# Optimization experiments

Measured on AMD Instinct MI355X. Metric: run time of the kernel, lower is better.

Reference implementation:

```python
import jax, jax.numpy as jnp
import numpy as np

T, B, H = 2048, 8, 1024


def setup_inputs() -> dict:
    key = jax.random.key(0)
    ks = jax.random.split(key, 4)
    scale = 1.0 / np.sqrt(H)
    x = jax.random.normal(ks[0], (T, B, H), dtype=jnp.float32)
    W_q = jax.random.normal(ks[1], (H, H), dtype=jnp.float32) * scale
    b_q = jnp.zeros((H,), dtype=jnp.float32)
    beta_raw = jax.random.normal(ks[2], (H,), dtype=jnp.float32)
    W_fc = jax.random.normal(ks[3], (H, H), dtype=jnp.float32) * scale
    b_fc = jnp.zeros((H,), dtype=jnp.float32)
    return {"x": x, "W_q": W_q, "b_q": b_q, "beta_raw": beta_raw,
            "W_fc": W_fc, "b_fc": b_fc}


def reference(x, W_q, b_q, beta_raw, W_fc, b_fc):
    # Per-neuron learned leak in (0,1)
    beta = jax.nn.sigmoid(beta_raw)  # (H,)
    # Input (q) projection: (T,B,H) @ (H,H)^T
    q = jnp.einsum('tbh,oh->tbo', x, W_q) + b_q  # (T,B,H)
    # Leaky integration m_t = beta * m_{t-1} + q_t as an associative scan over T
    a = jnp.broadcast_to(beta, q.shape)  # (T,B,H)

    def combine(c1, c2):
        a1, m1 = c1
        a2, m2 = c2
        return (a1 * a2, a2 * m1 + m2)

    _, m = jax.lax.associative_scan(combine, (a, q), axis=0)  # (T,B,H)
    # Linear + ReLU
    h = jnp.einsum('tbh,oh->tbo', m, W_fc) + b_fc
    return jax.nn.relu(h)
```

## Files before the change

### kernel.cpp

```cpp
#include <hip/hip_runtime.h>
#include <stdint.h>

typedef unsigned short u16;
typedef __bf16 bf16x8 __attribute__((ext_vector_type(8)));
typedef float f32x4 __attribute__((ext_vector_type(4)));

__device__ __forceinline__ u16 f2bf(float f) {
  union { float f; uint32_t u; } x; x.f = f;
  uint32_t u = x.u;
  u += 0x7fffu + ((u >> 16) & 1u);
  return (u16)(u >> 16);
}
__device__ __forceinline__ float bf2f(uint32_t lo16) {
  union { uint32_t u; float f; } x; x.u = lo16 << 16; return x.f;
}

__device__ __forceinline__ void async_load16(const u16* g, u16* l) {
  __builtin_amdgcn_global_load_lds(
      (const __attribute__((address_space(1))) void*)g,
      (__attribute__((address_space(3))) void*)l,
      16, 0, 0);
}

__global__ __launch_bounds__(256) void prep_all(const float* __restrict__ x,
                                                const float* __restrict__ Wq,
                                                const float* __restrict__ Wfc,
                                                const float* __restrict__ braw,
                                                u16* __restrict__ xb,
                                                u16* __restrict__ wqb,
                                                u16* __restrict__ wfcb,
                                                float* __restrict__ beta) {
  int gid = blockIdx.x * 256 + threadIdx.x;
  if (gid < 1024) beta[gid] = 1.0f / (1.0f + expf(-braw[gid]));
  if (gid < 131072) {
    const int HH = 1024 * 1024;
    int i = gid * 16;
    const float* src = (i < HH) ? (Wq + i) : (Wfc + (i - HH));
    u16* dst = (i < HH) ? (wqb + i) : (wfcb + (i - HH));
#pragma unroll
    for (int c = 0; c < 4; c++) {
      float4 v = *(const float4*)(src + c * 4);
      ushort4 o = {f2bf(v.x), f2bf(v.y), f2bf(v.z), f2bf(v.w)};
      *(ushort4*)(dst + c * 4) = o;
    }
  }
  {
    int i = gid * 8;
    float4 a = *(const float4*)(x + i);
    float4 b = *(const float4*)(x + i + 4);
    ushort4 o0 = {f2bf(a.x), f2bf(a.y), f2bf(a.z), f2bf(a.w)};
    ushort4 o1 = {f2bf(b.x), f2bf(b.y), f2bf(b.z), f2bf(b.w)};
    *(ushort4*)(xb + i) = o0;
    *(ushort4*)(xb + i + 4) = o1;
  }
}

template <int RELU, int OUTBF>
__global__ __launch_bounds__(512, 2) void gemm256(const u16* __restrict__ A,
                                                  const u16* __restrict__ B,
                                                  const float* __restrict__ bias,
                                                  void* __restrict__ Cout,
                                                  int M, int N, int K) {
  __shared__ u16 lds[4][2][256 * 32];

  const int tid  = threadIdx.x;
  const int lane = tid & 63;
  const int wid  = tid >> 6;
  const int wr   = (wid >> 2) * 128;
  const int wc   = (wid & 3) * 64;

  const int bid    = blockIdx.x;
  const int tile_m = (bid >> 2) * 256;
  const int tile_n = (bid & 3) * 256;

  const int srow    = tid >> 2;
  const int schunk  = (tid & 3) ^ ((srow >> 1) & 3);
  const u16* gA = A + (size_t)(tile_m + srow) * K + schunk * 8;
  const u16* gB = B + (size_t)(tile_n + srow) * K + schunk * 8;
  const size_t half_stride = (size_t)128 * K;

#define STAGE(slot, kt)                                                   \
  do {                                                                    \
    const size_t k0 = (size_t)(kt) * 32;                                  \
    async_load16(gA + k0,               &lds[slot][0][wid * 512]);        \
    async_load16(gA + k0 + half_stride, &lds[slot][0][4096 + wid * 512]); \
    async_load16(gB + k0,               &lds[slot][1][wid * 512]);        \
    async_load16(gB + k0 + half_stride, &lds[slot][1][4096 + wid * 512]); \
  } while (0)

  f32x4 acc[8][4];
#pragma unroll
  for (int i = 0; i < 8; i++)
#pragma unroll
    for (int j = 0; j < 4; j++) acc[i][j] = (f32x4){0.f, 0.f, 0.f, 0.f};

  const int lrow = lane & 15;
  const int kq   = lane >> 4;
  const int kc   = (lrow >> 1) & 3;
  const int coff = ((kq ^ kc) << 3);

  const int NKT = K >> 5;

  STAGE(0, 0);
  if (NKT > 1) STAGE(1, 1);
  if (NKT > 2) STAGE(2, 2);
  if (NKT > 2)      asm volatile("s_waitcnt vmcnt(8)" ::: "memory");
  else if (NKT > 1) asm volatile("s_waitcnt vmcnt(4)" ::: "memory");
  else              asm volatile("s_waitcnt vmcnt(0)" ::: "memory");
  __builtin_amdgcn_s_barrier();

  for (int kt = 0; kt < NKT; ++kt) {
    const int slot = kt & 3;
    const u16* As = &lds[slot][0][0];
    const u16* Bs = &lds[slot][1][0];

    bf16x8 a[8], b[4];
#pragma unroll
    for (int i = 0; i < 8; i++)
      a[i] = *(const bf16x8*)&As[(wr + i * 16 + lrow) * 32 + coff];
#pragma unroll
    for (int j = 0; j < 4; j++)
      b[j] = *(const bf16x8*)&Bs[(wc + j * 16 + lrow) * 32 + coff];

    if (kt + 3 < NKT) STAGE((kt + 3) & 3, kt + 3);

    __builtin_amdgcn_s_setprio(1);
#pragma unroll
    for (int i = 0; i < 8; i++)
#pragma unroll
      for (int j = 0; j < 4; j++)
        acc[i][j] = __builtin_amdgcn_mfma_f32_16x16x32_bf16(a[i], b[j], acc[i][j], 0, 0, 0);
    __builtin_amdgcn_s_setprio(0);

    const int ahead = NKT - 1 - kt;
    if (ahead >= 3) {
      asm volatile("s_waitcnt vmcnt(8)" ::: "memory");
      __builtin_amdgcn_s_barrier();
    } else if (ahead == 2) {
      asm volatile("s_waitcnt vmcnt(4)" ::: "memory");
      __builtin_amdgcn_s_barrier();
    } else if (ahead == 1) {
      asm volatile("s_waitcnt vmcnt(0)" ::: "memory");
      __builtin_amdgcn_s_barrier();
    }
  }
#undef STAGE

  const int crow = (lane >> 4) << 2;
  const int ccol = lane & 15;
#pragma unroll
  for (int i = 0; i < 8; i++) {
#pragma unroll
    for (int j = 0; j < 4; j++) {
      const int gm = tile_m + wr + i * 16 + crow;
      const int gn = tile_n + wc + j * 16 + ccol;
      const float bv = bias[gn];
#pragma unroll
      for (int r = 0; r < 4; r++) {
        float v = acc[i][j][r] + bv;
        if (RELU) v = fmaxf(v, 0.f);
        if (OUTBF) ((u16*)Cout)[(size_t)(gm + r) * N + gn] = f2bf(v);
        else       ((float*)Cout)[(size_t)(gm + r) * N + gn] = v;
      }
    }
  }
}

#define NCH 8192
#define SEG 32
#define NSEG 64

__global__ __launch_bounds__(256) void scan_carry(const uint2* __restrict__ qb,
                                                  float* __restrict__ carry,
                                                  const float* __restrict__ beta_arr) {
  int tid = blockIdx.x * 256 + threadIdx.x;
  int seg = tid >> 11;
  int cq  = tid & 2047;
  int h0  = (cq * 4) & 1023;
  float b0 = beta_arr[h0], b1 = beta_arr[h0 + 1], b2 = beta_arr[h0 + 2], b3 = beta_arr[h0 + 3];
  const uint2* p = qb + (size_t)seg * SEG * 2048 + cq;
  float m0 = 0.f, m1 = 0.f, m2 = 0.f, m3 = 0.f;
#pragma unroll 8
  for (int t = 0; t < SEG; t++) {
    uint2 v = p[(size_t)t * 2048];
    m0 = fmaf(b0, m0, bf2f(v.x & 0xffffu));
    m1 = fmaf(b1, m1, bf2f(v.x >> 16));
    m2 = fmaf(b2, m2, bf2f(v.y & 0xffffu));
    m3 = fmaf(b3, m3, bf2f(v.y >> 16));
  }
  *(float4*)&carry[(size_t)seg * NCH + cq * 4] = make_float4(m0, m1, m2, m3);
}

__global__ __launch_bounds__(256) void scan_fuse(const uint2* __restrict__ qb,
                                                 const float4* __restrict__ carry4,
                                                 const float* __restrict__ beta_arr,
                                                 uint2* __restrict__ mb) {
  const int tid = blockIdx.x * 256 + threadIdx.x;
  const int seg = tid >> 11;
  const int cq  = tid & 2047;
  const int h0  = (cq * 4) & 1023;
  const float b0 = beta_arr[h0], b1 = beta_arr[h0 + 1];
  const float b2 = beta_arr[h0 + 2], b3 = beta_arr[h0 + 3];
  float s0 = b0, s1 = b1, s2 = b2, s3 = b3;
#pragma unroll
  for (int i = 0; i < 5; i++) { s0 *= s0; s1 *= s1; s2 *= s2; s3 *= s3; }
  float m0 = 0.f, m1 = 0.f, m2 = 0.f, m3 = 0.f;
  const float4* cp = carry4 + cq;
  for (int s = 0; s < seg; s++) {
    float4 c = cp[(size_t)s * 2048];
    m0 = fmaf(s0, m0, c.x); m1 = fmaf(s1, m1, c.y);
    m2 = fmaf(s2, m2, c.z); m3 = fmaf(s3, m3, c.w);
  }
  const uint2* p = qb + (size_t)seg * SEG * 2048 + cq;
  uint2* o = mb + (size_t)seg * SEG * 2048 + cq;
#pragma unroll 8
  for (int t = 0; t < SEG; t++) {
    uint2 v = p[(size_t)t * 2048];
    m0 = fmaf(b0, m0, bf2f(v.x & 0xffffu));
    m1 = fmaf(b1, m1, bf2f(v.x >> 16));
    m2 = fmaf(b2, m2, bf2f(v.y & 0xffffu));
    m3 = fmaf(b3, m3, bf2f(v.y >> 16));
    uint2 w;
    w.x = (uint32_t)f2bf(m0) | ((uint32_t)f2bf(m1) << 16);
    w.y = (uint32_t)f2bf(m2) | ((uint32_t)f2bf(m3) << 16);
    o[(size_t)t * 2048] = w;
  }
}

extern "C" void kernel_launch(void* const* d_in, const int* in_sizes, int n_in,
                              void* d_out, int out_size, void* d_ws, size_t ws_size,
                              hipStream_t stream) {
  const float* x        = (const float*)d_in[0];
  const float* W_q      = (const float*)d_in[1];
  const float* b_q      = (const float*)d_in[2];
  const float* beta_raw = (const float*)d_in[3];
  const float* W_fc     = (const float*)d_in[4];
  const float* b_fc     = (const float*)d_in[5];

  const int H = 1024;
  const int M = 2048 * 8;
  const size_t MH = (size_t)M * H;

  char* ws = (char*)d_ws;
  u16* x_bf    = (u16*)ws;  ws += MH * 2;
  u16* q_bf    = (u16*)ws;  ws += MH * 2;
  u16* m_bf    = (u16*)ws;  ws += MH * 2;
  u16* wq_bf   = (u16*)ws;  ws += (size_t)H * H * 2;
  u16* wfc_bf  = (u16*)ws;  ws += (size_t)H * H * 2;
  float* beta  = (float*)ws; ws += 4096;
  float* carry = (float*)ws; ws += (size_t)NSEG * NCH * 4;

  prep_all<<<(int)(MH / 8 / 256), 256, 0, stream>>>(x, W_q, W_fc, beta_raw,
                                                    x_bf, wq_bf, wfc_bf, beta);

  gemm256<0, 1><<<256, 512, 0, stream>>>(x_bf, wq_bf, b_q, q_bf, M, H, H);

  scan_carry<<<NSEG * (NCH / 4) / 256, 256, 0, stream>>>((const uint2*)q_bf, carry, beta);
  scan_fuse<<<NSEG * (NCH / 4) / 256, 256, 0, stream>>>((const uint2*)q_bf,
                                                        (const float4*)carry, beta,
                                                        (uint2*)m_bf);

  gemm256<1, 0><<<256, 512, 0, stream>>>(m_bf, wfc_bf, b_fc, d_out, M, H, H);
}
```

Baseline: 240.1 us.

## Restructure GEMM main loop into 64-wide K tiles with interleaved sub-phase staging

The GEMM kernel moves from a 4-slot K=32 pipeline to a double-buffered K=64 pipeline. Each K tile is split into four phases that interleave A-fragment LDS reads, async global-to-LDS staging of the next A and B tiles, and MFMA blocks. The aim is to hide global and LDS latency behind the MFMA work. It also uses an 8-chunk XOR swizzle suited to 64-wide rows, and remaps block IDs so that tiles sharing an A row block land on the same XCD for better L2 reuse. The cost is many more barriers per iteration, and the tighter staging schedule could stall if loads do not arrive in time.

```diff
diff --git a/kernel.cpp b/kernel.cpp
--- a/kernel.cpp
+++ b/kernel.cpp
@@ -61,7 +61,7 @@
                                                   const float* __restrict__ bias,
                                                   void* __restrict__ Cout,
                                                   int M, int N, int K) {
-  __shared__ u16 lds[4][2][256 * 32];
+  __shared__ u16 lds[2][2][256 * 64];
 
   const int tid  = threadIdx.x;
   const int lane = tid & 63;
@@ -70,22 +70,29 @@
   const int wc   = (wid & 3) * 64;
 
   const int bid    = blockIdx.x;
-  const int tile_m = (bid >> 2) * 256;
-  const int tile_n = (bid & 3) * 256;
-
-  const int srow    = tid >> 2;
-  const int schunk  = (tid & 3) ^ ((srow >> 1) & 3);
-  const u16* gA = A + (size_t)(tile_m + srow) * K + schunk * 8;
-  const u16* gB = B + (size_t)(tile_n + srow) * K + schunk * 8;
-  const size_t half_stride = (size_t)128 * K;
-
-#define STAGE(slot, kt)                                                   \
-  do {                                                                    \
-    const size_t k0 = (size_t)(kt) * 32;                                  \
-    async_load16(gA + k0,               &lds[slot][0][wid * 512]);        \
-    async_load16(gA + k0 + half_stride, &lds[slot][0][4096 + wid * 512]); \
-    async_load16(gB + k0,               &lds[slot][1][wid * 512]);        \
-    async_load16(gB + k0 + half_stride, &lds[slot][1][4096 + wid * 512]); \
+  const int xcd    = bid & 7;
+  const int idx    = bid >> 3;
+  const int tile_m = ((xcd << 3) | (idx >> 2)) * 256;
+  const int tile_n = (idx & 3) * 256;
+
+  const int srow = tid >> 3;
+  const int sch  = (tid & 7) ^ (srow & 7);
+  const u16* gA = A + (size_t)(tile_m + srow) * K + sch * 8;
+  const u16* gB = B + (size_t)(tile_n + srow) * K + sch * 8;
+
+#define STAGE_A(bp, h, kt)                                              \
+  do {                                                                  \
+    const u16* _s = gA + (size_t)(h) * 128 * K + (size_t)(kt) * 64;     \
+    async_load16(_s,                 &(bp)[(h) * 8192 + wid * 512]);    \
+    async_load16(_s + (size_t)64 * K,                                   \
+                 &(bp)[(h) * 8192 + 4096 + wid * 512]);                 \
+  } while (0)
+#define STAGE_B(bp, h, kt)                                              \
+  do {                                                                  \
+    const u16* _s = gB + (size_t)(h) * 128 * K + (size_t)(kt) * 64;     \
+    async_load16(_s,                 &(bp)[(h) * 8192 + wid * 512]);    \
+    async_load16(_s + (size_t)64 * K,                                   \
+                 &(bp)[(h) * 8192 + 4096 + wid * 512]);                 \
   } while (0)
 
   f32x4 acc[8][4];
@@ -96,55 +103,136 @@
 
   const int lrow = lane & 15;
   const int kq   = lane >> 4;
-  const int kc   = (lrow >> 1) & 3;
-  const int coff = ((kq ^ kc) << 3);
-
-  const int NKT = K >> 5;
-
-  STAGE(0, 0);
-  if (NKT > 1) STAGE(1, 1);
-  if (NKT > 2) STAGE(2, 2);
-  if (NKT > 2)      asm volatile("s_waitcnt vmcnt(8)" ::: "memory");
-  else if (NKT > 1) asm volatile("s_waitcnt vmcnt(4)" ::: "memory");
-  else              asm volatile("s_waitcnt vmcnt(0)" ::: "memory");
+  const int x0   = ((kq)     ^ (lrow & 7)) << 3;
+  const int x1   = ((kq + 4) ^ (lrow & 7)) << 3;
+
+  const int NT = K >> 6;
+
+  {
+    u16* b0A = &lds[0][0][0];
+    u16* b0B = &lds[0][1][0];
+    STAGE_B(b0B, 0, 0);
+    STAGE_B(b0B, 1, 0);
+    STAGE_A(b0A, 0, 0);
+    STAGE_A(b0A, 1, 0);
+    if (NT > 1) {
+      u16* b1B = &lds[1][1][0];
+      STAGE_B(b1B, 0, 1);
+      STAGE_B(b1B, 1, 1);
+      asm volatile("s_waitcnt vmcnt(4)" ::: "memory");
+    } else {
+      asm volatile("s_waitcnt vmcnt(0)" ::: "memory");
+    }
+  }
   __builtin_amdgcn_s_barrier();
 
-  for (int kt = 0; kt < NKT; ++kt) {
-    const int slot = kt & 3;
-    const u16* As = &lds[slot][0][0];
-    const u16* Bs = &lds[slot][1][0];
-
-    bf16x8 a[8], b[4];
-#pragma unroll
-    for (int i = 0; i < 8; i++)
-      a[i] = *(const bf16x8*)&As[(wr + i * 16 + lrow) * 32 + coff];
-#pragma unroll
-    for (int j = 0; j < 4; j++)
-      b[j] = *(const bf16x8*)&Bs[(wc + j * 16 + lrow) * 32 + coff];
-
-    if (kt + 3 < NKT) STAGE((kt + 3) & 3, kt + 3);
-
+  bf16x8 bfr[4][2];
+
+  for (int t = 0; t < NT; ++t) {
+    const int buf = t & 1;
+    const u16* As = &lds[buf][0][0];
+    const u16* Bs = &lds[buf][1][0];
+    u16* nA = &lds[buf ^ 1][0][0];
+    u16* cB = &lds[buf][1][0];
+
+#pragma unroll
+    for (int n = 0; n < 4; n++) {
+      bfr[n][0] = *(const bf16x8*)&Bs[(wc + n * 16 + lrow) * 64 + x0];
+      bfr[n][1] = *(const bf16x8*)&Bs[(wc + n * 16 + lrow) * 64 + x1];
+    }
+    bf16x8 a0k0 = *(const bf16x8*)&As[(wr + 0 * 16 + lrow) * 64 + x0];
+    bf16x8 a0k1 = *(const bf16x8*)&As[(wr + 0 * 16 + lrow) * 64 + x1];
+    bf16x8 a1k0 = *(const bf16x8*)&As[(wr + 1 * 16 + lrow) * 64 + x0];
+    bf16x8 a1k1 = *(const bf16x8*)&As[(wr + 1 * 16 + lrow) * 64 + x1];
+    if (t + 1 < NT) { STAGE_A(nA, 0, t + 1); STAGE_A(nA, 1, t + 1); }
+    __builtin_amdgcn_s_barrier();
+    asm volatile("s_waitcnt lgkmcnt(0)" ::: "memory");
+    __builtin_amdgcn_sched_barrier(0);
     __builtin_amdgcn_s_setprio(1);
 #pragma unroll
-    for (int i = 0; i < 8; i++)
-#pragma unroll
-      for (int j = 0; j < 4; j++)
-        acc[i][j] = __builtin_amdgcn_mfma_f32_16x16x32_bf16(a[i], b[j], acc[i][j], 0, 0, 0);
+    for (int n = 0; n < 4; n++) {
+      acc[0][n] = __builtin_amdgcn_mfma_f32_16x16x32_bf16(a0k0, bfr[n][0], acc[0][n], 0, 0, 0);
+      acc[1][n] = __builtin_amdgcn_mfma_f32_16x16x32_bf16(a1k0, bfr[n][0], acc[1][n], 0, 0, 0);
+    }
+#pragma unroll
+    for (int n = 0; n < 4; n++) {
+      acc[0][n] = __builtin_amdgcn_mfma_f32_16x16x32_bf16(a0k1, bfr[n][1], acc[0][n], 0, 0, 0);
+      acc[1][n] = __builtin_amdgcn_mfma_f32_16x16x32_bf16(a1k1, bfr[n][1], acc[1][n], 0, 0, 0);
+    }
     __builtin_amdgcn_s_setprio(0);
-
-    const int ahead = NKT - 1 - kt;
-    if (ahead >= 3) {
-      asm volatile("s_waitcnt vmcnt(8)" ::: "memory");
-      __builtin_amdgcn_s_barrier();
-    } else if (ahead == 2) {
-      asm volatile("s_waitcnt vmcnt(4)" ::: "memory");
-      __builtin_amdgcn_s_barrier();
-    } else if (ahead == 1) {
-      asm volatile("s_waitcnt vmcnt(0)" ::: "memory");
-      __builtin_amdgcn_s_barrier();
-    }
-  }
-#undef STAGE
+    __builtin_amdgcn_s_barrier();
+
+    a0k0 = *(const bf16x8*)&As[(wr + 2 * 16 + lrow) * 64 + x0];
+    a0k1 = *(const bf16x8*)&As[(wr + 2 * 16 + lrow) * 64 + x1];
+    a1k0 = *(const bf16x8*)&As[(wr + 3 * 16 + lrow) * 64 + x0];
+    a1k1 = *(const bf16x8*)&As[(wr + 3 * 16 + lrow) * 64 + x1];
+    if (t + 2 < NT) STAGE_B(cB, 0, t + 2);
+    __builtin_amdgcn_s_barrier();
+    asm volatile("s_waitcnt lgkmcnt(0)" ::: "memory");
+    __builtin_amdgcn_sched_barrier(0);
+    __builtin_amdgcn_s_setprio(1);
+#pragma unroll
+    for (int n = 0; n < 4; n++) {
+      acc[2][n] = __builtin_amdgcn_mfma_f32_16x16x32_bf16(a0k0, bfr[n][0], acc[2][n], 0, 0, 0);
+      acc[3][n] = __builtin_amdgcn_mfma_f32_16x16x32_bf16(a1k0, bfr[n][0], acc[3][n], 0, 0, 0);
+    }
+#pragma unroll
+    for (int n = 0; n < 4; n++) {
+      acc[2][n] = __builtin_amdgcn_mfma_f32_16x16x32_bf16(a0k1, bfr[n][1], acc[2][n], 0, 0, 0);
+      acc[3][n] = __builtin_amdgcn_mfma_f32_16x16x32_bf16(a1k1, bfr[n][1], acc[3][n], 0, 0, 0);
+    }
+    __builtin_amdgcn_s_setprio(0);
+    __builtin_amdgcn_s_barrier();
+
+    a0k0 = *(const bf16x8*)&As[(wr + 4 * 16 + lrow) * 64 + x0];
+    a0k1 = *(const bf16x8*)&As[(wr + 4 * 16 + lrow) * 64 + x1];
+    a1k0 = *(const bf16x8*)&As[(wr + 5 * 16 + lrow) * 64 + x0];
+    a1k1 = *(const bf16x8*)&As[(wr + 5 * 16 + lrow) * 64 + x1];
+    if (t + 2 < NT) STAGE_B(cB, 1, t + 2);
+    __builtin_amdgcn_s_barrier();
+    asm volatile("s_waitcnt lgkmcnt(0)" ::: "memory");
+    __builtin_amdgcn_sched_barrier(0);
+    __builtin_amdgcn_s_setprio(1);
+#pragma unroll
+    for (int n = 0; n < 4; n++) {
+      acc[4][n] = __builtin_amdgcn_mfma_f32_16x16x32_bf16(a0k0, bfr[n][0], acc[4][n], 0, 0, 0);
+      acc[5][n] = __builtin_amdgcn_mfma_f32_16x16x32_bf16(a1k0, bfr[n][0], acc[5][n], 0, 0, 0);
+    }
+#pragma unroll
+    for (int n = 0; n < 4; n++) {
+      acc[4][n] = __builtin_amdgcn_mfma_f32_16x16x32_bf16(a0k1, bfr[n][1], acc[4][n], 0, 0, 0);
+      acc[5][n] = __builtin_amdgcn_mfma_f32_16x16x32_bf16(a1k1, bfr[n][1], acc[5][n], 0, 0, 0);
+    }
+    __builtin_amdgcn_s_setprio(0);
+    __builtin_amdgcn_s_barrier();
+
+    a0k0 = *(const bf16x8*)&As[(wr + 6 * 16 + lrow) * 64 + x0];
+    a0k1 = *(const bf16x8*)&As[(wr + 6 * 16 + lrow) * 64 + x1];
+    a1k0 = *(const bf16x8*)&As[(wr + 7 * 16 + lrow) * 64 + x0];
+    a1k1 = *(const bf16x8*)&As[(wr + 7 * 16 + lrow) * 64 + x1];
+    if (t < NT - 1) {
+      if (t + 2 < NT) asm volatile("s_waitcnt vmcnt(4)" ::: "memory");
+      else            asm volatile("s_waitcnt vmcnt(0)" ::: "memory");
+    }
+    __builtin_amdgcn_s_barrier();
+    asm volatile("s_waitcnt lgkmcnt(0)" ::: "memory");
+    __builtin_amdgcn_sched_barrier(0);
+    __builtin_amdgcn_s_setprio(1);
+#pragma unroll
+    for (int n = 0; n < 4; n++) {
+      acc[6][n] = __builtin_amdgcn_mfma_f32_16x16x32_bf16(a0k0, bfr[n][0], acc[6][n], 0, 0, 0);
+      acc[7][n] = __builtin_amdgcn_mfma_f32_16x16x32_bf16(a1k0, bfr[n][0], acc[7][n], 0, 0, 0);
+    }
+#pragma unroll
+    for (int n = 0; n < 4; n++) {
+      acc[6][n] = __builtin_amdgcn_mfma_f32_16x16x32_bf16(a0k1, bfr[n][1], acc[6][n], 0, 0, 0);
+      acc[7][n] = __builtin_amdgcn_mfma_f32_16x16x32_bf16(a1k1, bfr[n][1], acc[7][n], 0, 0, 0);
+    }
+    __builtin_amdgcn_s_setprio(0);
+    if (t < NT - 1) __builtin_amdgcn_s_barrier();
+  }
+#undef STAGE_A
+#undef STAGE_B
 
   const int crow = (lane >> 4) << 2;
   const int ccol = lane & 15;
```

Result: no change. 237.7 us (-1.0%).

## Load B fragments directly to registers, double-buffer A in LDS with BK=64, XCD tile remap

Applied to the files above, without the earlier changes.

Restructures the bf16 GEMM main loop. The B operand is now prefetched straight from global memory into registers, one step ahead, and no longer goes through LDS. The A tile is double-buffered in LDS with a 64-wide K step and an 8-way XOR swizzle, where before there was a 4-slot ring with K=32. Block IDs are remapped so that each XCD gets a contiguous range of M tiles, which should improve L2 locality. The aim is to cut LDS traffic and barriers per K step, at the cost of redundant global/L2 reads of B across waves and a shallower prefetch depth.

```diff
diff --git a/kernel.cpp b/kernel.cpp
--- a/kernel.cpp
+++ b/kernel.cpp
@@ -61,7 +61,7 @@
                                                   const float* __restrict__ bias,
                                                   void* __restrict__ Cout,
                                                   int M, int N, int K) {
-  __shared__ u16 lds[4][2][256 * 32];
+  __shared__ u16 lds[2][256 * 64];
 
   const int tid  = threadIdx.x;
   const int lane = tid & 63;
@@ -70,22 +70,22 @@
   const int wc   = (wid & 3) * 64;
 
   const int bid    = blockIdx.x;
-  const int tile_m = (bid >> 2) * 256;
-  const int tile_n = (bid & 3) * 256;
-
-  const int srow    = tid >> 2;
-  const int schunk  = (tid & 3) ^ ((srow >> 1) & 3);
-  const u16* gA = A + (size_t)(tile_m + srow) * K + schunk * 8;
-  const u16* gB = B + (size_t)(tile_n + srow) * K + schunk * 8;
-  const size_t half_stride = (size_t)128 * K;
-
-#define STAGE(slot, kt)                                                   \
-  do {                                                                    \
-    const size_t k0 = (size_t)(kt) * 32;                                  \
-    async_load16(gA + k0,               &lds[slot][0][wid * 512]);        \
-    async_load16(gA + k0 + half_stride, &lds[slot][0][4096 + wid * 512]); \
-    async_load16(gB + k0,               &lds[slot][1][wid * 512]);        \
-    async_load16(gB + k0 + half_stride, &lds[slot][1][4096 + wid * 512]); \
+  const int xcd    = bid & 7;
+  const int idx    = bid >> 3;
+  const int tile_m = ((xcd << 3) | (idx >> 2)) * 256;
+  const int tile_n = (idx & 3) * 256;
+
+  const int srow = tid >> 3;
+  const int sch  = (tid & 7) ^ (srow & 7);
+  const u16* gA = A + (size_t)(tile_m + srow) * K + sch * 8;
+
+#define STAGE_A(bp, kt)                                                \
+  do {                                                                 \
+    const u16* _s = gA + (size_t)(kt) * 64;                            \
+    async_load16(_s,                   &(bp)[wid * 512]);              \
+    async_load16(_s + (size_t)64 * K,  &(bp)[4096 + wid * 512]);       \
+    async_load16(_s + (size_t)128 * K, &(bp)[8192 + wid * 512]);       \
+    async_load16(_s + (size_t)192 * K, &(bp)[12288 + wid * 512]);      \
   } while (0)
 
   f32x4 acc[8][4];
@@ -96,55 +96,62 @@
 
   const int lrow = lane & 15;
   const int kq   = lane >> 4;
-  const int kc   = (lrow >> 1) & 3;
-  const int coff = ((kq ^ kc) << 3);
-
-  const int NKT = K >> 5;
-
-  STAGE(0, 0);
-  if (NKT > 1) STAGE(1, 1);
-  if (NKT > 2) STAGE(2, 2);
-  if (NKT > 2)      asm volatile("s_waitcnt vmcnt(8)" ::: "memory");
-  else if (NKT > 1) asm volatile("s_waitcnt vmcnt(4)" ::: "memory");
-  else              asm volatile("s_waitcnt vmcnt(0)" ::: "memory");
+  const int x0   = ((kq)     ^ (lrow & 7)) << 3;
+  const int x1   = ((kq + 4) ^ (lrow & 7)) << 3;
+
+  const u16* gBf = B + (size_t)(tile_n + wc + lrow) * K + kq * 8;
+
+  const int NT = K >> 6;
+
+  bf16x8 bA[4][2], bB[4][2];
+
+  STAGE_A(lds[0], 0);
+  __builtin_amdgcn_sched_barrier(0);
+#pragma unroll
+  for (int n = 0; n < 4; n++) {
+    bA[n][0] = *(const bf16x8*)(gBf + (size_t)n * 16 * K);
+    bA[n][1] = *(const bf16x8*)(gBf + (size_t)n * 16 * K + 32);
+  }
+  __builtin_amdgcn_sched_barrier(0);
+  asm volatile("s_waitcnt vmcnt(8)" ::: "memory");
   __builtin_amdgcn_s_barrier();
 
-  for (int kt = 0; kt < NKT; ++kt) {
-    const int slot = kt & 3;
-    const u16* As = &lds[slot][0][0];
-    const u16* Bs = &lds[slot][1][0];
-
-    bf16x8 a[8], b[4];
-#pragma unroll
-    for (int i = 0; i < 8; i++)
-      a[i] = *(const bf16x8*)&As[(wr + i * 16 + lrow) * 32 + coff];
-#pragma unroll
-    for (int j = 0; j < 4; j++)
-      b[j] = *(const bf16x8*)&Bs[(wc + j * 16 + lrow) * 32 + coff];
-
-    if (kt + 3 < NKT) STAGE((kt + 3) & 3, kt + 3);
-
-    __builtin_amdgcn_s_setprio(1);
-#pragma unroll
-    for (int i = 0; i < 8; i++)
-#pragma unroll
-      for (int j = 0; j < 4; j++)
-        acc[i][j] = __builtin_amdgcn_mfma_f32_16x16x32_bf16(a[i], b[j], acc[i][j], 0, 0, 0);
-    __builtin_amdgcn_s_setprio(0);
-
-    const int ahead = NKT - 1 - kt;
-    if (ahead >= 3) {
+  auto iter = [&](int t, u16* __restrict__ Ac, u16* __restrict__ An,
+                  bf16x8 (&bc)[4][2], bf16x8 (&bn)[4][2]) {
+    const int t1 = t + 1;
+    if (t1 < NT) STAGE_A(An, t1);
+    __builtin_amdgcn_sched_barrier(0);
+    if (t1 < NT) {
+#pragma unroll
+      for (int n = 0; n < 4; n++) {
+        bn[n][0] = *(const bf16x8*)(gBf + (size_t)n * 16 * K + (size_t)t1 * 64);
+        bn[n][1] = *(const bf16x8*)(gBf + (size_t)n * 16 * K + (size_t)t1 * 64 + 32);
+      }
+    }
+    __builtin_amdgcn_sched_barrier(0);
+#pragma unroll
+    for (int i = 0; i < 8; i++) {
+      bf16x8 a0 = *(const bf16x8*)&Ac[(wr + i * 16 + lrow) * 64 + x0];
+      bf16x8 a1 = *(const bf16x8*)&Ac[(wr + i * 16 + lrow) * 64 + x1];
+#pragma unroll
+      for (int n = 0; n < 4; n++) {
+        acc[i][n] = __builtin_amdgcn_mfma_f32_16x16x32_bf16(a0, bc[n][0], acc[i][n], 0, 0, 0);
+        acc[i][n] = __builtin_amdgcn_mfma_f32_16x16x32_bf16(a1, bc[n][1], acc[i][n], 0, 0, 0);
+      }
+    }
+    if (t1 < NT) {
+      asm volatile("s_waitcnt lgkmcnt(0)" ::: "memory");
+      __builtin_amdgcn_sched_barrier(0);
       asm volatile("s_waitcnt vmcnt(8)" ::: "memory");
       __builtin_amdgcn_s_barrier();
-    } else if (ahead == 2) {
-      asm volatile("s_waitcnt vmcnt(4)" ::: "memory");
-      __builtin_amdgcn_s_barrier();
-    } else if (ahead == 1) {
-      asm volatile("s_waitcnt vmcnt(0)" ::: "memory");
-      __builtin_amdgcn_s_barrier();
-    }
-  }
-#undef STAGE
+    }
+  };
+
+  for (int t = 0; t < NT; t += 2) {
+    iter(t, lds[0], lds[1], bA, bB);
+    if (t + 1 < NT) iter(t + 1, lds[1], lds[0], bB, bA);
+  }
+#undef STAGE_A
 
   const int crow = (lane >> 4) << 2;
   const int ccol = lane & 15;
```

Result: slower. 264.5 us (+10.1%).

## Fuse scan segment-carry computation into q-projection GEMM epilogue and remap tiles per XCD

Applied to the files above, without the earlier changes.

The q-projection GEMM epilogue now computes each 32-timestep segment's local scan carry directly from the fp32 accumulators: it weights rows by powers of beta, reduces across lanes and warps via shuffles and LDS, and writes the carry array. The separate scan_carry kernel, which re-read the whole bf16 q tensor, is removed. Block-to-tile mapping is also remapped so that consecutive M tiles land on the same XCD for better L2 locality. This adds epilogue work and an extra sync to the GEMM, and the carry is now computed from unrounded fp32 values instead of the bf16 q.

```diff
diff --git a/kernel.cpp b/kernel.cpp
--- a/kernel.cpp
+++ b/kernel.cpp
@@ -55,11 +55,13 @@
   }
 }
 
-template <int RELU, int OUTBF>
+template <int RELU, int OUTBF, int CARRY>
 __global__ __launch_bounds__(512, 2) void gemm256(const u16* __restrict__ A,
                                                   const u16* __restrict__ B,
                                                   const float* __restrict__ bias,
                                                   void* __restrict__ Cout,
+                                                  const float* __restrict__ beta_arr,
+                                                  float* __restrict__ carry_out,
                                                   int M, int N, int K) {
   __shared__ u16 lds[4][2][256 * 32];
 
@@ -70,8 +72,10 @@
   const int wc   = (wid & 3) * 64;
 
   const int bid    = blockIdx.x;
-  const int tile_m = (bid >> 2) * 256;
-  const int tile_n = (bid & 3) * 256;
+  const int xcd    = bid & 7;
+  const int idx    = bid >> 3;
+  const int tile_m = ((xcd << 3) | (idx >> 2)) * 256;
+  const int tile_n = (idx & 3) * 256;
 
   const int srow    = tid >> 2;
   const int schunk  = (tid & 3) ^ ((srow >> 1) & 3);
@@ -164,32 +168,48 @@
       }
     }
   }
+
+  if (CARRY) {
+    float* ps = (float*)&lds[0][0][0];
+    const int W   = wr >> 7;
+    const int kap = lane >> 5;
+#pragma unroll
+    for (int j = 0; j < 4; j++) {
+      const int gn = tile_n + wc + j * 16 + ccol;
+      const float bv = bias[gn];
+      const float b1 = beta_arr[gn];
+      const float b2 = b1 * b1;
+      const float b4 = b2 * b2, b8 = b4 * b4, b16 = b8 * b8;
+      const float scale = W ? (kap ? 1.0f : b1) : (kap ? b16 : b16 * b1);
+#pragma unroll
+      for (int r = 0; r < 4; r++) {
+        float Hn = acc[0][j][r] + bv;
+#pragma unroll
+        for (int i = 1; i < 8; i++) Hn = fmaf(b2, Hn, acc[i][j][r] + bv);
+        float P = scale * Hn;
+        P += __shfl_xor(P, 32);
+        if (lane < 32) {
+          const int bb = ((lane >> 4) << 2) + r;
+          ps[W * 2048 + bb * 256 + wc + j * 16 + ccol] = P;
+        }
+      }
+    }
+    __syncthreads();
+    {
+      const int bb = tid >> 6;
+      const int h4 = (tid & 63) << 2;
+      float4 lo = *(float4*)&ps[bb * 256 + h4];
+      float4 hi = *(float4*)&ps[2048 + bb * 256 + h4];
+      float4 s  = make_float4(lo.x + hi.x, lo.y + hi.y, lo.z + hi.z, lo.w + hi.w);
+      const int seg = tile_m >> 8;
+      *(float4*)&carry_out[(size_t)seg * 8192 + bb * 1024 + tile_n + h4] = s;
+    }
+  }
 }
 
 #define NCH 8192
 #define SEG 32
 #define NSEG 64
-
-__global__ __launch_bounds__(256) void scan_carry(const uint2* __restrict__ qb,
-                                                  float* __restrict__ carry,
-                                                  const float* __restrict__ beta_arr) {
-  int tid = blockIdx.x * 256 + threadIdx.x;
-  int seg = tid >> 11;
-  int cq  = tid & 2047;
-  int h0  = (cq * 4) & 1023;
-  float b0 = beta_arr[h0], b1 = beta_arr[h0 + 1], b2 = beta_arr[h0 + 2], b3 = beta_arr[h0 + 3];
-  const uint2* p = qb + (size_t)seg * SEG * 2048 + cq;
-  float m0 = 0.f, m1 = 0.f, m2 = 0.f, m3 = 0.f;
-#pragma unroll 8
-  for (int t = 0; t < SEG; t++) {
-    uint2 v = p[(size_t)t * 2048];
-    m0 = fmaf(b0, m0, bf2f(v.x & 0xffffu));
-    m1 = fmaf(b1, m1, bf2f(v.x >> 16));
-    m2 = fmaf(b2, m2, bf2f(v.y & 0xffffu));
-    m3 = fmaf(b3, m3, bf2f(v.y >> 16));
-  }
-  *(float4*)&carry[(size_t)seg * NCH + cq * 4] = make_float4(m0, m1, m2, m3);
-}
 
 __global__ __launch_bounds__(256) void scan_fuse(const uint2* __restrict__ qb,
                                                  const float4* __restrict__ carry4,
@@ -253,12 +273,13 @@
   prep_all<<<(int)(MH / 8 / 256), 256, 0, stream>>>(x, W_q, W_fc, beta_raw,
                                                     x_bf, wq_bf, wfc_bf, beta);
 
-  gemm256<0, 1><<<256, 512, 0, stream>>>(x_bf, wq_bf, b_q, q_bf, M, H, H);
-
-  scan_carry<<<NSEG * (NCH / 4) / 256, 256, 0, stream>>>((const uint2*)q_bf, carry, beta);
+  gemm256<0, 1, 1><<<256, 512, 0, stream>>>(x_bf, wq_bf, b_q, q_bf,
+                                            beta, carry, M, H, H);
+
   scan_fuse<<<NSEG * (NCH / 4) / 256, 256, 0, stream>>>((const uint2*)q_bf,
                                                         (const float4*)carry, beta,
                                                         (uint2*)m_bf);
 
-  gemm256<1, 0><<<256, 512, 0, stream>>>(m_bf, wfc_bf, b_fc, d_out, M, H, H);
-}
+  gemm256<1, 0, 0><<<256, 512, 0, stream>>>(m_bf, wfc_bf, b_fc, d_out,
+                                            beta, nullptr, M, H, H);
+}
```

Result: faster. 234.4 us (median of 2 runs) (-2.4%).
